# Optimization experiments

Hardware: AMD Instinct MI355X
Metric: run time of the kernel (lower is better)

The kernel has to match this reference:

```python
import jax, jax.numpy as jnp
import numpy as np

B, N, D, L, K = 8, 1024, 256, 512, 16
T0, T1, N_STEPS = 0.0, 0.2, 8  # fixed-step RK4 in place of torchdiffeq implicit_adams


def setup_inputs() -> dict:
    key = jax.random.key(0)
    k1, k2, k3 = jax.random.split(key, 3)
    tokens = jax.random.normal(k1, (B, N, D), dtype=jnp.float32)
    x_bn = jax.random.normal(k2, (B, N, L), dtype=jnp.float32)
    theta_W = jax.random.normal(k3, (D, D), dtype=jnp.float32) * 0.02  # nn.Linear weight [out,in]
    alpha_raw = jnp.asarray(0.1, dtype=jnp.float32)
    return {"tokens": tokens, "x_bn": x_bn, "theta_W": theta_W, "alpha_raw": alpha_raw}


def _pearson_corr(x_bn):
    # x_bn: [B,N,L] -> corr [B,N,N]; torch .std() is unbiased (ddof=1)
    Ln = x_bn.shape[-1]
    x = x_bn - x_bn.mean(axis=-1, keepdims=True)
    x = x / (x.std(axis=-1, ddof=1, keepdims=True) + 1e-6)
    return jnp.matmul(x, x.swapaxes(-1, -2)) / (Ln - 1)


def _build_topk_A(corr, k):
    b, n, _ = corr.shape
    idx = jax.lax.top_k(corr, k + 1)[1]                      # [B,N,k+1]
    bi = jnp.arange(b)[:, None, None]
    ni = jnp.arange(n)[None, :, None]
    mask = jnp.zeros_like(corr).at[bi, ni, idx].set(1.0)
    A = corr * mask
    A = (A + A.swapaxes(-1, -2)) * 0.5
    A = A + jnp.eye(n, dtype=A.dtype)[None]
    deg = jnp.maximum(A.sum(-1), 1e-6)                       # [B,N]
    Dinv = deg ** -0.5
    return Dinv[:, :, None] * A * Dinv[:, None, :]


def reference(tokens, x_bn, theta_W, alpha_raw):
    corr = _pearson_corr(x_bn)
    A = _build_topk_A(corr, K)                               # [B,N,N]
    Lap = jnp.eye(N, dtype=A.dtype)[None] - A                # L = I - A
    alpha = jnp.minimum(jax.nn.softplus(alpha_raw), 2.0)

    def rhs(x):  # x: [B,N,D]
        diff = alpha * jnp.matmul(Lap, x)
        react = jnp.matmul(jnp.matmul(A, x), theta_W.T)      # Linear(no bias)
        return diff + react

    dt = jnp.asarray((T1 - T0) / N_STEPS, dtype=tokens.dtype)

    def step(x, _):
        k1 = rhs(x)
        k2 = rhs(x + 0.5 * dt * k1)
        k3 = rhs(x + 0.5 * dt * k2)
        k4 = rhs(x + dt * k3)
        return x + (dt / 6.0) * (k1 + 2.0 * k2 + 2.0 * k3 + k4), None

    y, _ = jax.lax.scan(step, tokens, None, length=N_STEPS)
    return jax.nn.relu(y)
```

## Files before the change

### kernel.cpp

```cpp
#include <hip/hip_runtime.h>
#include <math.h>

#define BB 8
#define NN 1024
#define DD 256
#define LL 512
#define KK 16
#define NROWS (BB*NN)
#define MAXNZ 128
#define NTERM 4

__global__ __launch_bounds__(64) void k_stats(const float* __restrict__ x,
                                              float* __restrict__ xhat) {
  int row = blockIdx.x;
  int l = threadIdx.x;
  const float* xr = x + (size_t)row * LL;
  float4 a = *reinterpret_cast<const float4*>(xr + l * 8);
  float4 b = *reinterpret_cast<const float4*>(xr + l * 8 + 4);
  float s = a.x + a.y + a.z + a.w + b.x + b.y + b.z + b.w;
  float sq = a.x*a.x + a.y*a.y + a.z*a.z + a.w*a.w +
             b.x*b.x + b.y*b.y + b.z*b.z + b.w*b.w;
  for (int off = 32; off >= 1; off >>= 1) {
    s  += __shfl_xor(s, off);
    sq += __shfl_xor(sq, off);
  }
  float mean = s * (1.0f / LL);
  float var = (sq - (float)LL * mean * mean) * (1.0f / (LL - 1));
  var = fmaxf(var, 0.0f);
  float inv = 1.0f / (sqrtf(var) + 1e-6f);
  float4 oa, ob;
  oa.x = (a.x - mean) * inv; oa.y = (a.y - mean) * inv;
  oa.z = (a.z - mean) * inv; oa.w = (a.w - mean) * inv;
  ob.x = (b.x - mean) * inv; ob.y = (b.y - mean) * inv;
  ob.z = (b.z - mean) * inv; ob.w = (b.w - mean) * inv;
  float* orow = xhat + (size_t)row * LL;
  *reinterpret_cast<float4*>(orow + l * 8)     = oa;
  *reinterpret_cast<float4*>(orow + l * 8 + 4) = ob;
}

__global__ __launch_bounds__(256) void k_corr(const float* __restrict__ xh,
                                              float* __restrict__ corr) {
  __shared__ float As[2][16][68];
  __shared__ float Bs[2][16][68];
  int b = blockIdx.x & 7;
  int t = blockIdx.x >> 3;
  int ti = 0, off = t;
  while (off >= 16 - ti) { off -= 16 - ti; ++ti; }
  int tj = ti + off;
  int i0 = ti * 64, j0 = tj * 64;
  int tid = threadIdx.x;
  int tr = tid >> 4, tc = tid & 15;
  int li = tid >> 2, lk = (tid & 3) * 4;
  const float* xb = xh + (size_t)b * NN * LL;
  const float* arow = xb + (size_t)(i0 + li) * LL + lk;
  const float* brow = xb + (size_t)(j0 + li) * LL + lk;

  {
    float4 va = *reinterpret_cast<const float4*>(arow);
    float4 vb = *reinterpret_cast<const float4*>(brow);
    As[0][lk + 0][li] = va.x; As[0][lk + 1][li] = va.y;
    As[0][lk + 2][li] = va.z; As[0][lk + 3][li] = va.w;
    Bs[0][lk + 0][li] = vb.x; Bs[0][lk + 1][li] = vb.y;
    Bs[0][lk + 2][li] = vb.z; Bs[0][lk + 3][li] = vb.w;
  }
  __syncthreads();

  float c[4][4] = {{0}};
  int cur = 0;
  for (int k0 = 0; k0 < LL; k0 += 16) {
    float4 na, nb;
    bool has_next = (k0 + 16 < LL);
    if (has_next) {
      na = *reinterpret_cast<const float4*>(arow + k0 + 16);
      nb = *reinterpret_cast<const float4*>(brow + k0 + 16);
    }
#pragma unroll
    for (int kk = 0; kk < 16; ++kk) {
      float4 av = *reinterpret_cast<const float4*>(&As[cur][kk][tr * 4]);
      float4 bv = *reinterpret_cast<const float4*>(&Bs[cur][kk][tc * 4]);
      c[0][0] = fmaf(av.x, bv.x, c[0][0]); c[0][1] = fmaf(av.x, bv.y, c[0][1]);
      c[0][2] = fmaf(av.x, bv.z, c[0][2]); c[0][3] = fmaf(av.x, bv.w, c[0][3]);
      c[1][0] = fmaf(av.y, bv.x, c[1][0]); c[1][1] = fmaf(av.y, bv.y, c[1][1]);
      c[1][2] = fmaf(av.y, bv.z, c[1][2]); c[1][3] = fmaf(av.y, bv.w, c[1][3]);
      c[2][0] = fmaf(av.z, bv.x, c[2][0]); c[2][1] = fmaf(av.z, bv.y, c[2][1]);
      c[2][2] = fmaf(av.z, bv.z, c[2][2]); c[2][3] = fmaf(av.z, bv.w, c[2][3]);
      c[3][0] = fmaf(av.w, bv.x, c[3][0]); c[3][1] = fmaf(av.w, bv.y, c[3][1]);
      c[3][2] = fmaf(av.w, bv.z, c[3][2]); c[3][3] = fmaf(av.w, bv.w, c[3][3]);
    }
    if (has_next) {
      int nxt = cur ^ 1;
      As[nxt][lk + 0][li] = na.x; As[nxt][lk + 1][li] = na.y;
      As[nxt][lk + 2][li] = na.z; As[nxt][lk + 3][li] = na.w;
      Bs[nxt][lk + 0][li] = nb.x; Bs[nxt][lk + 1][li] = nb.y;
      Bs[nxt][lk + 2][li] = nb.z; Bs[nxt][lk + 3][li] = nb.w;
      __syncthreads();
      cur = nxt;
    }
  }

  const float inv = 1.0f / (float)(LL - 1);
  float* cb = corr + (size_t)b * NN * NN;
#pragma unroll
  for (int r = 0; r < 4; ++r) {
    float4 o;
    o.x = c[r][0] * inv; o.y = c[r][1] * inv; o.z = c[r][2] * inv; o.w = c[r][3] * inv;
    *reinterpret_cast<float4*>(cb + (size_t)(i0 + tr * 4 + r) * NN + j0 + tc * 4) = o;
  }
  if (ti != tj) {
#pragma unroll
    for (int r = 0; r < 4; ++r) {
#pragma unroll
      for (int cc = 0; cc < 4; ++cc)
        cb[(size_t)(j0 + tc * 4 + cc) * NN + i0 + tr * 4 + r] = c[r][cc] * inv;
    }
  }
}

__global__ __launch_bounds__(64) void k_topk(const float* __restrict__ corr,
                                             int* __restrict__ tcols,
                                             float* __restrict__ tvals) {
  int row = blockIdx.x;
  int l = threadIdx.x;
  const float* cr = corr + (size_t)row * NN;
  float v[16];
#pragma unroll
  for (int m = 0; m < 16; ++m) v[m] = cr[m * 64 + l];
  for (int it = 0; it < KK + 1; ++it) {
    float bv = v[0]; int bm = 0;
#pragma unroll
    for (int m = 1; m < 16; ++m)
      if (v[m] > bv) { bv = v[m]; bm = m; }
    int bc = bm * 64 + l;
    for (int off = 32; off >= 1; off >>= 1) {
      float ov = __shfl_xor(bv, off);
      int oc = __shfl_xor(bc, off);
      if (ov > bv || (ov == bv && oc < bc)) { bv = ov; bc = oc; }
    }
    if ((bc & 63) == l) v[bc >> 6] = -__builtin_inff();
    if (l == 0) { tcols[row * 17 + it] = bc; tvals[row * 17 + it] = bv; }
  }
}

__global__ void k_scatter(const int* __restrict__ tcols,
                          const float* __restrict__ tvals,
                          float* __restrict__ A) {
  int t = blockIdx.x * 256 + threadIdx.x;
  const int NT = NROWS * 17;
  if (t < NT) {
    int row = t / 17;
    int b = row >> 10, i = row & 1023;
    int j = tcols[t];
    float hv = 0.5f * tvals[t];
    atomicAdd(A + (size_t)row * NN + j, hv);
    atomicAdd(A + ((size_t)b * NN + j) * NN + i, hv);
  } else if (t < NT + NROWS) {
    int row = t - NT;
    atomicAdd(A + (size_t)row * NN + (row & 1023), 1.0f);
  }
}

__global__ __launch_bounds__(64) void k_deg(const float* __restrict__ A,
                                            float* __restrict__ Dinv) {
  int row = blockIdx.x;
  int l = threadIdx.x;
  const float* ar = A + (size_t)row * NN;
  float s = 0.0f;
#pragma unroll
  for (int m = 0; m < 16; ++m) s += ar[m * 64 + l];
  for (int off = 32; off >= 1; off >>= 1) s += __shfl_xor(s, off);
  if (l == 0) Dinv[row] = 1.0f / sqrtf(fmaxf(s, 1e-6f));
}

__global__ __launch_bounds__(64) void k_compact(const float* __restrict__ A,
                                                const float* __restrict__ Dinv,
                                                int* __restrict__ cnt,
                                                int* __restrict__ colsA,
                                                float* __restrict__ valsA) {
  int row = blockIdx.x;
  int l = threadIdx.x;
  int b = row >> 10;
  const float* ar = A + (size_t)row * NN;
  float di = Dinv[row];
  int base = 0;
  for (int m = 0; m < 16; ++m) {
    int colj = m * 64 + l;
    float a = ar[colj];
    bool nz = (a != 0.0f);
    unsigned long long mask = __ballot(nz);
    int pos = base + __popcll(mask & ((1ull << l) - 1ull));
    if (nz && pos < MAXNZ) {
      colsA[(size_t)row * MAXNZ + pos] = colj;
      valsA[(size_t)row * MAXNZ + pos] = a * di * Dinv[b * NN + colj];
    }
    base += __popcll(mask);
  }
  if (l == 0) cnt[row] = base < MAXNZ ? base : MAXNZ;
}

__global__ void k_buildM(const float* __restrict__ W,
                         const float* __restrict__ araw,
                         float* __restrict__ M,
                         float* __restrict__ dcoef) {
  float a = araw[0];
  float alpha = fminf(log1pf(expf(a)), 2.0f);
  int t = blockIdx.x * 256 + threadIdx.x;
  int k = t >> 8, d = t & 255;
  M[t] = W[d * DD + k] - (k == d ? alpha : 0.0f);
  if (t == 0) {
    const double h = 0.2 / 8.0;
    double B0 = h * (double)alpha, B1 = h;
    double T[NTERM + 1];
    for (int i = 0; i <= NTERM; ++i) T[i] = 0.0;
    T[0] = 1.0 + B0 * 0.25; T[1] = B1 * 0.25;
    for (int kk = 3; kk >= 1; --kk) {
      double U[NTERM + 1];
      double c0 = B0 / kk, c1 = B1 / kk;
      for (int i = 0; i <= NTERM; ++i)
        U[i] = c0 * T[i] + (i ? c1 * T[i - 1] : 0.0);
      U[0] += 1.0;
      for (int i = 0; i <= NTERM; ++i) T[i] = U[i];
    }
    double P2[NTERM + 1], P4[NTERM + 1], G[NTERM + 1];
    for (int i = 0; i <= NTERM; ++i) {
      double s = 0; for (int j = 0; j <= i; ++j) s += T[j] * T[i - j]; P2[i] = s;
    }
    for (int i = 0; i <= NTERM; ++i) {
      double s = 0; for (int j = 0; j <= i; ++j) s += P2[j] * P2[i - j]; P4[i] = s;
    }
    for (int i = 0; i <= NTERM; ++i) {
      double s = 0; for (int j = 0; j <= i; ++j) s += P4[j] * P4[i - j]; G[i] = s;
    }
    for (int i = 0; i <= NTERM; ++i) dcoef[i] = (float)G[i];
  }
}

__global__ __launch_bounds__(256) void k_gather(const float* __restrict__ xin,
                                                float* __restrict__ y,
                                                const int* __restrict__ cnt,
                                                const int* __restrict__ cols,
                                                const float* __restrict__ vals) {
  int p = blockIdx.x;
  int b = p & 7;
  int tile = p >> 3;
  int w = threadIdx.x >> 6, l = threadIdx.x & 63;
  int row = tile * 4 + w;
  int grow = b * NN + row;
  const float* xb = xin + (size_t)b * NN * DD;
  int c = cnt[grow];
  const int* cp = cols + (size_t)grow * MAXNZ;
  const float* vp = vals + (size_t)grow * MAXNZ;
  float4 acc = {0.0f, 0.0f, 0.0f, 0.0f};
  for (int base = 0; base < c; base += 64) {
    int ci = 0; float vi = 0.0f;
    if (base + l < c) { ci = cp[base + l]; vi = vp[base + l]; }
    int m = c - base; if (m > 64) m = 64;
#pragma unroll 8
    for (int s = 0; s < m; ++s) {
      int colj = __shfl(ci, s);
      float v = __shfl(vi, s);
      float4 xv = *reinterpret_cast<const float4*>(xb + (size_t)colj * DD + l * 4);
      acc.x = fmaf(v, xv.x, acc.x);
      acc.y = fmaf(v, xv.y, acc.y);
      acc.z = fmaf(v, xv.z, acc.z);
      acc.w = fmaf(v, xv.w, acc.w);
    }
  }
  *reinterpret_cast<float4*>(y + (size_t)grow * DD + l * 4) = acc;
}

__global__ __launch_bounds__(256) void k_term(const float* __restrict__ y,
                                              const float* __restrict__ M,
                                              const float* __restrict__ tokens,
                                              float* __restrict__ vout,
                                              float* __restrict__ out,
                                              const float* __restrict__ dcoef,
                                              int iterm, int last) {
  __shared__ __align__(16) float yT[DD][20];
  int p = blockIdx.x;
  int b = p & 7;
  int tile = p >> 3;
  int row0 = tile * 16;
  int tid = threadIdx.x;
  {
    int lr = tid >> 4, kq = (tid & 15) * 16;
    const float* yr = y + ((size_t)(b * NN + row0 + lr)) * DD + kq;
#pragma unroll
    for (int j4 = 0; j4 < 4; ++j4) {
      float4 v = *reinterpret_cast<const float4*>(yr + j4 * 4);
      yT[kq + j4 * 4 + 0][lr] = v.x;
      yT[kq + j4 * 4 + 1][lr] = v.y;
      yT[kq + j4 * 4 + 2][lr] = v.z;
      yT[kq + j4 * 4 + 3][lr] = v.w;
    }
  }
  __syncthreads();

  int w = tid >> 6, l = tid & 63;
  int col = w * 64 + l;
  float acc[16];
#pragma unroll
  for (int r = 0; r < 16; ++r) acc[r] = 0.0f;
  const float* Mc = M + col;
#pragma unroll 4
  for (int k = 0; k < DD; ++k) {
    float mv = Mc[k * DD];
    const float4* yr = reinterpret_cast<const float4*>(&yT[k][0]);
    float4 y0 = yr[0], y1 = yr[1], y2 = yr[2], y3 = yr[3];
    acc[0]  = fmaf(y0.x, mv, acc[0]);  acc[1]  = fmaf(y0.y, mv, acc[1]);
    acc[2]  = fmaf(y0.z, mv, acc[2]);  acc[3]  = fmaf(y0.w, mv, acc[3]);
    acc[4]  = fmaf(y1.x, mv, acc[4]);  acc[5]  = fmaf(y1.y, mv, acc[5]);
    acc[6]  = fmaf(y1.z, mv, acc[6]);  acc[7]  = fmaf(y1.w, mv, acc[7]);
    acc[8]  = fmaf(y2.x, mv, acc[8]);  acc[9]  = fmaf(y2.y, mv, acc[9]);
    acc[10] = fmaf(y2.z, mv, acc[10]); acc[11] = fmaf(y2.w, mv, acc[11]);
    acc[12] = fmaf(y3.x, mv, acc[12]); acc[13] = fmaf(y3.y, mv, acc[13]);
    acc[14] = fmaf(y3.z, mv, acc[14]); acc[15] = fmaf(y3.w, mv, acc[15]);
  }

  float sA = (iterm == 1) ? dcoef[NTERM] : 1.0f;
  float sB = dcoef[NTERM - iterm];
  size_t rowbase = (size_t)b * NN + row0;
#pragma unroll
  for (int r = 0; r < 16; ++r) {
    size_t gi = (rowbase + r) * DD + col;
    float val = fmaf(sB, tokens[gi], sA * acc[r]);
    if (last) out[gi] = fmaxf(val, 0.0f);
    else      vout[gi] = val;
  }
}

extern "C" void kernel_launch(void* const* d_in, const int* in_sizes, int n_in,
                              void* d_out, int out_size, void* d_ws, size_t ws_size,
                              hipStream_t stream) {
  const float* tokens = (const float*)d_in[0];
  const float* x_bn   = (const float*)d_in[1];
  const float* thetaW = (const float*)d_in[2];
  const float* araw   = (const float*)d_in[3];
  float* out = (float*)d_out;

  float* ws = (float*)d_ws;
  float* xhat  = ws;
  float* corrA = xhat + (size_t)4 * 1024 * 1024;
  float* tvals = corrA + (size_t)8 * 1024 * 1024;
  int*   tcols = (int*)(tvals + NROWS * 17);
  float* Dinv  = (float*)(tcols + NROWS * 17);
  float* Mmat  = Dinv + NROWS;
  float* dcoef = Mmat + DD * DD;
  int*   cnt   = (int*)(dcoef + 64);
  int*   colsA = cnt + NROWS;
  float* valsA = (float*)(colsA + NROWS * MAXNZ);
  float* t0   = corrA;
  float* t1   = t0 + (size_t)NROWS * DD;
  float* ybuf = t1 + (size_t)NROWS * DD;

  k_stats<<<NROWS, 64, 0, stream>>>(x_bn, xhat);
  k_corr<<<136 * 8, 256, 0, stream>>>(xhat, corrA);
  k_topk<<<NROWS, 64, 0, stream>>>(corrA, tcols, tvals);
  hipMemsetAsync(corrA, 0, (size_t)8 * 1024 * 1024 * sizeof(float), stream);
  k_scatter<<<(NROWS * 17 + NROWS + 255) / 256, 256, 0, stream>>>(tcols, tvals, corrA);
  k_deg<<<NROWS, 64, 0, stream>>>(corrA, Dinv);
  k_compact<<<NROWS, 64, 0, stream>>>(corrA, Dinv, cnt, colsA, valsA);
  k_buildM<<<DD * DD / 256, 256, 0, stream>>>(thetaW, araw, Mmat, dcoef);

  const float* vin = tokens;
  for (int i = 1; i <= NTERM; ++i) {
    k_gather<<<2048, 256, 0, stream>>>(vin, ybuf, cnt, colsA, valsA);
    float* vo = (i & 1) ? t0 : t1;
    k_term<<<512, 256, 0, stream>>>(ybuf, Mmat, tokens, vo, out, dcoef,
                                    i, i == NTERM ? 1 : 0);
    vin = vo;
  }
}
```

Before: 371.8 us.

## Build sparse adjacency directly via atomic CSR append and fuse gather with dense term

```diff
diff --git a/kernel.cpp b/kernel.cpp
--- a/kernel.cpp
+++ b/kernel.cpp
@@ -118,7 +118,8 @@
 
 __global__ __launch_bounds__(64) void k_topk(const float* __restrict__ corr,
                                              int* __restrict__ tcols,
-                                             float* __restrict__ tvals) {
+                                             float* __restrict__ tvals,
+                                             int* __restrict__ cnt) {
   int row = blockIdx.x;
   int l = threadIdx.x;
   const float* cr = corr + (size_t)row * NN;
@@ -139,11 +140,14 @@
     if ((bc & 63) == l) v[bc >> 6] = -__builtin_inff();
     if (l == 0) { tcols[row * 17 + it] = bc; tvals[row * 17 + it] = bv; }
   }
-}
-
-__global__ void k_scatter(const int* __restrict__ tcols,
-                          const float* __restrict__ tvals,
-                          float* __restrict__ A) {
+  if (l == 0) cnt[row] = 0;
+}
+
+__global__ void k_csr(const int* __restrict__ tcols,
+                      const float* __restrict__ tvals,
+                      int* __restrict__ cnt,
+                      int* __restrict__ colsA,
+                      float* __restrict__ valsA) {
   int t = blockIdx.x * 256 + threadIdx.x;
   const int NT = NROWS * 17;
   if (t < NT) {
@@ -151,50 +155,53 @@
     int b = row >> 10, i = row & 1023;
     int j = tcols[t];
     float hv = 0.5f * tvals[t];
-    atomicAdd(A + (size_t)row * NN + j, hv);
-    atomicAdd(A + ((size_t)b * NN + j) * NN + i, hv);
+    int gj = b * NN + j;
+    int p1 = atomicAdd(&cnt[row], 1);
+    if (p1 < MAXNZ) {
+      colsA[(size_t)row * MAXNZ + p1] = j;
+      valsA[(size_t)row * MAXNZ + p1] = hv;
+    }
+    int p2 = atomicAdd(&cnt[gj], 1);
+    if (p2 < MAXNZ) {
+      colsA[(size_t)gj * MAXNZ + p2] = i;
+      valsA[(size_t)gj * MAXNZ + p2] = hv;
+    }
   } else if (t < NT + NROWS) {
     int row = t - NT;
-    atomicAdd(A + (size_t)row * NN + (row & 1023), 1.0f);
-  }
-}
-
-__global__ __launch_bounds__(64) void k_deg(const float* __restrict__ A,
-                                            float* __restrict__ Dinv) {
+    int p = atomicAdd(&cnt[row], 1);
+    if (p < MAXNZ) {
+      colsA[(size_t)row * MAXNZ + p] = row & 1023;
+      valsA[(size_t)row * MAXNZ + p] = 1.0f;
+    }
+  }
+}
+
+__global__ __launch_bounds__(64) void k_deg2(const int* __restrict__ cnt,
+                                             const float* __restrict__ valsA,
+                                             float* __restrict__ Dinv) {
   int row = blockIdx.x;
   int l = threadIdx.x;
-  const float* ar = A + (size_t)row * NN;
+  int c = cnt[row]; c = c < MAXNZ ? c : MAXNZ;
+  const float* vp = valsA + (size_t)row * MAXNZ;
   float s = 0.0f;
-#pragma unroll
-  for (int m = 0; m < 16; ++m) s += ar[m * 64 + l];
+  for (int base = l; base < c; base += 64) s += vp[base];
   for (int off = 32; off >= 1; off >>= 1) s += __shfl_xor(s, off);
   if (l == 0) Dinv[row] = 1.0f / sqrtf(fmaxf(s, 1e-6f));
 }
 
-__global__ __launch_bounds__(64) void k_compact(const float* __restrict__ A,
-                                                const float* __restrict__ Dinv,
-                                                int* __restrict__ cnt,
-                                                int* __restrict__ colsA,
-                                                float* __restrict__ valsA) {
+__global__ __launch_bounds__(64) void k_norm(const int* __restrict__ cnt,
+                                             const int* __restrict__ colsA,
+                                             float* __restrict__ valsA,
+                                             const float* __restrict__ Dinv) {
   int row = blockIdx.x;
   int l = threadIdx.x;
   int b = row >> 10;
-  const float* ar = A + (size_t)row * NN;
+  int c = cnt[row]; c = c < MAXNZ ? c : MAXNZ;
   float di = Dinv[row];
-  int base = 0;
-  for (int m = 0; m < 16; ++m) {
-    int colj = m * 64 + l;
-    float a = ar[colj];
-    bool nz = (a != 0.0f);
-    unsigned long long mask = __ballot(nz);
-    int pos = base + __popcll(mask & ((1ull << l) - 1ull));
-    if (nz && pos < MAXNZ) {
-      colsA[(size_t)row * MAXNZ + pos] = colj;
-      valsA[(size_t)row * MAXNZ + pos] = a * di * Dinv[b * NN + colj];
-    }
-    base += __popcll(mask);
-  }
-  if (l == 0) cnt[row] = base < MAXNZ ? base : MAXNZ;
+  for (int base = l; base < c; base += 64) {
+    int j = colsA[(size_t)row * MAXNZ + base];
+    valsA[(size_t)row * MAXNZ + base] *= di * Dinv[b * NN + j];
+  }
 }
 
 __global__ void k_buildM(const float* __restrict__ W,
@@ -234,94 +241,77 @@
   }
 }
 
-__global__ __launch_bounds__(256) void k_gather(const float* __restrict__ xin,
-                                                float* __restrict__ y,
-                                                const int* __restrict__ cnt,
-                                                const int* __restrict__ cols,
-                                                const float* __restrict__ vals) {
+__global__ __launch_bounds__(256) void k_q(const float* __restrict__ vin,
+                                           const float* __restrict__ M,
+                                           const float* __restrict__ tokens,
+                                           float* __restrict__ vout,
+                                           float* __restrict__ out,
+                                           const int* __restrict__ cnt,
+                                           const int* __restrict__ colsA,
+                                           const float* __restrict__ valsA,
+                                           const float* __restrict__ dcoef,
+                                           int iterm, int last) {
+  __shared__ __align__(16) float ylds[8][DD];
   int p = blockIdx.x;
   int b = p & 7;
   int tile = p >> 3;
-  int w = threadIdx.x >> 6, l = threadIdx.x & 63;
-  int row = tile * 4 + w;
-  int grow = b * NN + row;
-  const float* xb = xin + (size_t)b * NN * DD;
-  int c = cnt[grow];
-  const int* cp = cols + (size_t)grow * MAXNZ;
-  const float* vp = vals + (size_t)grow * MAXNZ;
-  float4 acc = {0.0f, 0.0f, 0.0f, 0.0f};
-  for (int base = 0; base < c; base += 64) {
-    int ci = 0; float vi = 0.0f;
-    if (base + l < c) { ci = cp[base + l]; vi = vp[base + l]; }
-    int m = c - base; if (m > 64) m = 64;
+  int row0 = tile * 8;
+  int tid = threadIdx.x;
+  int w = tid >> 6, l = tid & 63;
+  const float* xb = vin + (size_t)b * NN * DD;
+
+  for (int rr = 0; rr < 2; ++rr) {
+    int lr = w * 2 + rr;
+    int grow = b * NN + row0 + lr;
+    int c = cnt[grow]; c = c < MAXNZ ? c : MAXNZ;
+    const int* cp = colsA + (size_t)grow * MAXNZ;
+    const float* vp = valsA + (size_t)grow * MAXNZ;
+    float4 acc = {0.0f, 0.0f, 0.0f, 0.0f};
+    for (int base = 0; base < c; base += 64) {
+      int ci = 0; float vi = 0.0f;
+      if (base + l < c) { ci = cp[base + l]; vi = vp[base + l]; }
+      int m = c - base; if (m > 64) m = 64;
 #pragma unroll 8
-    for (int s = 0; s < m; ++s) {
-      int colj = __shfl(ci, s);
-      float v = __shfl(vi, s);
-      float4 xv = *reinterpret_cast<const float4*>(xb + (size_t)colj * DD + l * 4);
-      acc.x = fmaf(v, xv.x, acc.x);
-      acc.y = fmaf(v, xv.y, acc.y);
-      acc.z = fmaf(v, xv.z, acc.z);
-      acc.w = fmaf(v, xv.w, acc.w);
-    }
-  }
-  *reinterpret_cast<float4*>(y + (size_t)grow * DD + l * 4) = acc;
-}
-
-__global__ __launch_bounds__(256) void k_term(const float* __restrict__ y,
-                                              const float* __restrict__ M,
-                                              const float* __restrict__ tokens,
-                                              float* __restrict__ vout,
-                                              float* __restrict__ out,
-                                              const float* __restrict__ dcoef,
-                                              int iterm, int last) {
-  __shared__ __align__(16) float yT[DD][20];
-  int p = blockIdx.x;
-  int b = p & 7;
-  int tile = p >> 3;
-  int row0 = tile * 16;
-  int tid = threadIdx.x;
-  {
-    int lr = tid >> 4, kq = (tid & 15) * 16;
-    const float* yr = y + ((size_t)(b * NN + row0 + lr)) * DD + kq;
-#pragma unroll
-    for (int j4 = 0; j4 < 4; ++j4) {
-      float4 v = *reinterpret_cast<const float4*>(yr + j4 * 4);
-      yT[kq + j4 * 4 + 0][lr] = v.x;
-      yT[kq + j4 * 4 + 1][lr] = v.y;
-      yT[kq + j4 * 4 + 2][lr] = v.z;
-      yT[kq + j4 * 4 + 3][lr] = v.w;
-    }
+      for (int s = 0; s < m; ++s) {
+        int colj = __shfl(ci, s);
+        float v = __shfl(vi, s);
+        float4 xv = *reinterpret_cast<const float4*>(xb + (size_t)colj * DD + l * 4);
+        acc.x = fmaf(v, xv.x, acc.x);
+        acc.y = fmaf(v, xv.y, acc.y);
+        acc.z = fmaf(v, xv.z, acc.z);
+        acc.w = fmaf(v, xv.w, acc.w);
+      }
+    }
+    *reinterpret_cast<float4*>(&ylds[lr][l * 4]) = acc;
   }
   __syncthreads();
 
-  int w = tid >> 6, l = tid & 63;
-  int col = w * 64 + l;
-  float acc[16];
-#pragma unroll
-  for (int r = 0; r < 16; ++r) acc[r] = 0.0f;
-  const float* Mc = M + col;
+  float acc[8];
+#pragma unroll
+  for (int r = 0; r < 8; ++r) acc[r] = 0.0f;
+  const float* Mc = M + tid;
 #pragma unroll 4
-  for (int k = 0; k < DD; ++k) {
-    float mv = Mc[k * DD];
-    const float4* yr = reinterpret_cast<const float4*>(&yT[k][0]);
-    float4 y0 = yr[0], y1 = yr[1], y2 = yr[2], y3 = yr[3];
-    acc[0]  = fmaf(y0.x, mv, acc[0]);  acc[1]  = fmaf(y0.y, mv, acc[1]);
-    acc[2]  = fmaf(y0.z, mv, acc[2]);  acc[3]  = fmaf(y0.w, mv, acc[3]);
-    acc[4]  = fmaf(y1.x, mv, acc[4]);  acc[5]  = fmaf(y1.y, mv, acc[5]);
-    acc[6]  = fmaf(y1.z, mv, acc[6]);  acc[7]  = fmaf(y1.w, mv, acc[7]);
-    acc[8]  = fmaf(y2.x, mv, acc[8]);  acc[9]  = fmaf(y2.y, mv, acc[9]);
-    acc[10] = fmaf(y2.z, mv, acc[10]); acc[11] = fmaf(y2.w, mv, acc[11]);
-    acc[12] = fmaf(y3.x, mv, acc[12]); acc[13] = fmaf(y3.y, mv, acc[13]);
-    acc[14] = fmaf(y3.z, mv, acc[14]); acc[15] = fmaf(y3.w, mv, acc[15]);
+  for (int k0 = 0; k0 < DD; k0 += 4) {
+    float m0 = Mc[(k0 + 0) * DD];
+    float m1 = Mc[(k0 + 1) * DD];
+    float m2 = Mc[(k0 + 2) * DD];
+    float m3 = Mc[(k0 + 3) * DD];
+#pragma unroll
+    for (int r = 0; r < 8; ++r) {
+      float4 y = *reinterpret_cast<const float4*>(&ylds[r][k0]);
+      acc[r] = fmaf(y.x, m0, acc[r]);
+      acc[r] = fmaf(y.y, m1, acc[r]);
+      acc[r] = fmaf(y.z, m2, acc[r]);
+      acc[r] = fmaf(y.w, m3, acc[r]);
+    }
   }
 
   float sA = (iterm == 1) ? dcoef[NTERM] : 1.0f;
   float sB = dcoef[NTERM - iterm];
   size_t rowbase = (size_t)b * NN + row0;
 #pragma unroll
-  for (int r = 0; r < 16; ++r) {
-    size_t gi = (rowbase + r) * DD + col;
+  for (int r = 0; r < 8; ++r) {
+    size_t gi = (rowbase + r) * DD + tid;
     float val = fmaf(sB, tokens[gi], sA * acc[r]);
     if (last) out[gi] = fmaxf(val, 0.0f);
     else      vout[gi] = val;
@@ -350,23 +340,21 @@
   float* valsA = (float*)(colsA + NROWS * MAXNZ);
   float* t0   = corrA;
   float* t1   = t0 + (size_t)NROWS * DD;
-  float* ybuf = t1 + (size_t)NROWS * DD;
 
   k_stats<<<NROWS, 64, 0, stream>>>(x_bn, xhat);
   k_corr<<<136 * 8, 256, 0, stream>>>(xhat, corrA);
-  k_topk<<<NROWS, 64, 0, stream>>>(corrA, tcols, tvals);
-  hipMemsetAsync(corrA, 0, (size_t)8 * 1024 * 1024 * sizeof(float), stream);
-  k_scatter<<<(NROWS * 17 + NROWS + 255) / 256, 256, 0, stream>>>(tcols, tvals, corrA);
-  k_deg<<<NROWS, 64, 0, stream>>>(corrA, Dinv);
-  k_compact<<<NROWS, 64, 0, stream>>>(corrA, Dinv, cnt, colsA, valsA);
+  k_topk<<<NROWS, 64, 0, stream>>>(corrA, tcols, tvals, cnt);
+  k_csr<<<(NROWS * 17 + NROWS + 255) / 256, 256, 0, stream>>>(tcols, tvals, cnt,
+                                                              colsA, valsA);
+  k_deg2<<<NROWS, 64, 0, stream>>>(cnt, valsA, Dinv);
+  k_norm<<<NROWS, 64, 0, stream>>>(cnt, colsA, valsA, Dinv);
   k_buildM<<<DD * DD / 256, 256, 0, stream>>>(thetaW, araw, Mmat, dcoef);
 
   const float* vin = tokens;
   for (int i = 1; i <= NTERM; ++i) {
-    k_gather<<<2048, 256, 0, stream>>>(vin, ybuf, cnt, colsA, valsA);
     float* vo = (i & 1) ? t0 : t1;
-    k_term<<<512, 256, 0, stream>>>(ybuf, Mmat, tokens, vo, out, dcoef,
-                                    i, i == NTERM ? 1 : 0);
+    k_q<<<1024, 256, 0, stream>>>(vin, Mmat, tokens, vo, out, cnt, colsA, valsA,
+                                  dcoef, i, i == NTERM ? 1 : 0);
     vin = vo;
   }
 }
```

Measured after the change: 373.8 us. No clear change (+0.5%).
